# Performance work log

Hardware: AMD Instinct MI355X
Metric: run time of the kernel (lower is better)

## Reference

```python
import jax, jax.numpy as jnp
import numpy as np

N = 1024
BATCH = 256


def setup_inputs() -> dict:
    key = jax.random.key(0)
    k1, k2 = jax.random.split(key)
    log_alpha = jax.random.normal(k1, (BATCH, N), dtype=jnp.float32)
    W = jax.random.normal(k2, (N, N), dtype=jnp.float32)  # unnormalized transition matrix
    return {"log_alpha": log_alpha, "W": W}


def reference(log_alpha, W):
    # log_softmax over dim=0 (columns are distributions over next state)
    log_T = jax.nn.log_softmax(W, axis=0)  # [N, N]
    # log_domain_matmul: out[i, m] = logsumexp_j( log_T[i, j] + log_alpha[m, j] )
    # then transpose back -> out[m, i]
    # broadcast-add cube [BATCH, N, N] then logsumexp over j (tropical-semiring matmul)
    out = jax.scipy.special.logsumexp(
        log_T[None, :, :] + log_alpha[:, None, :], axis=2
    )  # [BATCH, N]
    return out
```

## Files before the change

kernel.cpp:

```cpp
#include <hip/hip_runtime.h>
#include <hip/hip_bf16.h>

#define N 1024
#define BATCH 256
#define NSLAB 16

typedef __attribute__((ext_vector_type(8))) short short8;
typedef __attribute__((ext_vector_type(8))) float f32x8;
typedef __attribute__((ext_vector_type(4))) float f32x4;

static __device__ __forceinline__ ushort bfbits(float f) {
    union { __hip_bfloat16 h; ushort u; } cv;
    cv.h = __float2bfloat16(f);
    return cv.u;
}
static __device__ __forceinline__ float bf2f(ushort u) {
    union { ushort u; __hip_bfloat16 h; } cv;
    cv.u = u;
    return __bfloat162float(cv.h);
}

__global__ __launch_bounds__(256) void k1_psplit(const float* __restrict__ W,
                                                 float* __restrict__ psum,
                                                 __hip_bfloat16* __restrict__ Ph,
                                                 __hip_bfloat16* __restrict__ Pl) {
    const int t    = threadIdx.x;
    const int jg   = blockIdx.x & 15;
    const int slab = blockIdx.x >> 4;
    const int j    = jg * 64 + (t & 63);
    const int rb   = slab * 64 + (t >> 6);

    float acc = 0.f;
#pragma unroll 4
    for (int it = 0; it < 16; ++it) {
        const int i   = rb + it * 4;
        const float e = __expf(W[i * N + j]);
        const __hip_bfloat16 h = __float2bfloat16(e);
        Ph[i * N + j] = h;
        Pl[i * N + j] = __float2bfloat16(e - __bfloat162float(h));
        acc += e;
    }
    __shared__ float sm[256];
    sm[t] = acc;
    __syncthreads();
    if (t < 64)
        psum[slab * N + j] = sm[t] + sm[t + 64] + sm[t + 128] + sm[t + 192];
}

__global__ __launch_bounds__(256) void k3_fused(const float* __restrict__ la,
                                                const float* __restrict__ psum,
                                                const ushort* __restrict__ Ph,
                                                const ushort* __restrict__ Pl,
                                                float* __restrict__ out) {
    __shared__ float  lcs[N];
    __shared__ ushort sQh[32 * 72], sQl[32 * 72], sPh[32 * 72], sPl[32 * 72];

    const int t    = threadIdx.x;
    const int m0   = (blockIdx.x >> 5) * 32;
    const int i0   = (blockIdx.x & 31) * 32;
    const int lane = t & 63;
    const int wid  = t >> 6;
    const int wm   = wid >> 1;
    const int wn   = wid & 1;

#pragma unroll
    for (int jj = 0; jj < 4; ++jj) {
        const int j = jj * 256 + t;
        float cs = 0.f;
#pragma unroll
        for (int s = 0; s < NSLAB; ++s) cs += psum[s * N + j];
        lcs[j] = __logf(cs);
    }
    __syncthreads();

    const int srow = t >> 3;
    const int skc  = (t & 7) * 8;
    const float*  gla = la + (m0 + srow) * N + skc;
    const ushort* gPh = Ph + (i0 + srow) * N + skc;
    const ushort* gPl = Pl + (i0 + srow) * N + skc;
    const int sdst = srow * 72 + skc;

    const int frow = lane & 15;
    const int fkb  = (lane >> 4) * 8;
    const int aoff = (wm * 16 + frow) * 72 + fkb;
    const int boff = (wn * 16 + frow) * 72 + fkb;

    f32x4 acc = {0.f, 0.f, 0.f, 0.f};

    f32x8 vla = *(const f32x8*)(gla);
    short8 vph = *(const short8*)(gPh);
    short8 vpl = *(const short8*)(gPl);

    for (int k0 = 0; k0 < N; k0 += 64) {
        short8 qh, ql;
#pragma unroll
        for (int x = 0; x < 8; ++x) {
            const float q  = __expf(vla[x] - lcs[k0 + skc + x]);
            const ushort h = bfbits(q);
            qh[x] = (short)h;
            ql[x] = (short)bfbits(q - bf2f(h));
        }
        __syncthreads();
        *(short8*)&sQh[sdst] = qh;
        *(short8*)&sQl[sdst] = ql;
        *(short8*)&sPh[sdst] = vph;
        *(short8*)&sPl[sdst] = vpl;
        if (k0 + 64 < N) {
            vla = *(const f32x8*)(gla + k0 + 64);
            vph = *(const short8*)(gPh + k0 + 64);
            vpl = *(const short8*)(gPl + k0 + 64);
        }
        __syncthreads();
#pragma unroll
        for (int ks = 0; ks < 2; ++ks) {
            const short8 aQh = *(const short8*)&sQh[aoff + ks * 32];
            const short8 aQl = *(const short8*)&sQl[aoff + ks * 32];
            const short8 bPh = *(const short8*)&sPh[boff + ks * 32];
            const short8 bPl = *(const short8*)&sPl[boff + ks * 32];
            acc = __builtin_amdgcn_mfma_f32_16x16x32_bf16(aQh, bPh, acc, 0, 0, 0);
            acc = __builtin_amdgcn_mfma_f32_16x16x32_bf16(aQh, bPl, acc, 0, 0, 0);
            acc = __builtin_amdgcn_mfma_f32_16x16x32_bf16(aQl, bPh, acc, 0, 0, 0);
        }
    }

    const int om = m0 + wm * 16 + (lane >> 4) * 4;
    const int oi = i0 + wn * 16 + (lane & 15);
#pragma unroll
    for (int r = 0; r < 4; ++r)
        out[(om + r) * N + oi] = __logf(acc[r]);
}

extern "C" void kernel_launch(void* const* d_in, const int* in_sizes, int n_in,
                              void* d_out, int out_size, void* d_ws, size_t ws_size,
                              hipStream_t stream) {
    const float* la = (const float*)d_in[0];
    const float* W  = (const float*)d_in[1];
    float* out = (float*)d_out;

    char* ws = (char*)d_ws;
    float* psum        = (float*)ws;
    __hip_bfloat16* Ph = (__hip_bfloat16*)(ws + (64 << 10));
    __hip_bfloat16* Pl = Ph + (size_t)N * N;

    k1_psplit<<<256, 256, 0, stream>>>(W, psum, Ph, Pl);
    k3_fused<<<256, 256, 0, stream>>>(la, psum,
                                      (const ushort*)Ph, (const ushort*)Pl, out);
}
```

Before: 72.76 us.

## Split Q precompute into separate kernel and use split-K matmul with 512 threads

Moves the column-sum log and exp/bf16 hi-lo split of log_alpha out of the matmul kernel into a new k2_qsplit kernel, so each Q element is computed once instead of being recomputed by every i-block. The matmul kernel now loads precomputed bf16 Q tiles, uses 128-wide K tiles with 8 waves split across two K halves, and reduces the partial sums through shared memory. k1 is vectorized to 4-wide loads and stores with 16-row slabs. The cost is an extra kernel launch, an extra global round trip for Qh/Ql, and a 64-way psum reduction in k2.

```diff
diff --git a/kernel.cpp b/kernel.cpp
--- a/kernel.cpp
+++ b/kernel.cpp
@@ -3,112 +3,142 @@
 
 #define N 1024
 #define BATCH 256
-#define NSLAB 16
+#define LPAD 136
 
+typedef __attribute__((ext_vector_type(4))) short short4v;
 typedef __attribute__((ext_vector_type(8))) short short8;
-typedef __attribute__((ext_vector_type(8))) float f32x8;
 typedef __attribute__((ext_vector_type(4))) float f32x4;
 
 static __device__ __forceinline__ ushort bfbits(float f) {
-    union { __hip_bfloat16 h; ushort u; } cv;
-    cv.h = __float2bfloat16(f);
-    return cv.u;
+    union { __hip_bfloat16 h; ushort u; } cv; cv.h = __float2bfloat16(f); return cv.u;
 }
 static __device__ __forceinline__ float bf2f(ushort u) {
-    union { ushort u; __hip_bfloat16 h; } cv;
-    cv.u = u;
-    return __bfloat162float(cv.h);
+    union { ushort u; __hip_bfloat16 h; } cv; cv.u = u; return __bfloat162float(cv.h);
 }
 
 __global__ __launch_bounds__(256) void k1_psplit(const float* __restrict__ W,
                                                  float* __restrict__ psum,
-                                                 __hip_bfloat16* __restrict__ Ph,
-                                                 __hip_bfloat16* __restrict__ Pl) {
-    const int t    = threadIdx.x;
-    const int jg   = blockIdx.x & 15;
-    const int slab = blockIdx.x >> 4;
-    const int j    = jg * 64 + (t & 63);
-    const int rb   = slab * 64 + (t >> 6);
-
-    float acc = 0.f;
-#pragma unroll 4
-    for (int it = 0; it < 16; ++it) {
-        const int i   = rb + it * 4;
-        const float e = __expf(W[i * N + j]);
-        const __hip_bfloat16 h = __float2bfloat16(e);
-        Ph[i * N + j] = h;
-        Pl[i * N + j] = __float2bfloat16(e - __bfloat162float(h));
+                                                 ushort* __restrict__ Ph,
+                                                 ushort* __restrict__ Pl) {
+    const int t = threadIdx.x, lane = t & 63, w = t >> 6;
+    const int cg = blockIdx.x & 3, slab = blockIdx.x >> 2;
+    const int c = cg * 256 + lane * 4;
+    __shared__ f32x4 sm[4][64];
+    f32x4 acc = {0.f, 0.f, 0.f, 0.f};
+#pragma unroll
+    for (int it = 0; it < 4; ++it) {
+        const int row = slab * 16 + w * 4 + it;
+        const f32x4 v = *(const f32x4*)(W + row * N + c);
+        short4v ph, pl;
+        f32x4 e;
+#pragma unroll
+        for (int x = 0; x < 4; ++x) {
+            e[x] = __expf(v[x]);
+            const ushort h = bfbits(e[x]);
+            ph[x] = (short)h;
+            pl[x] = (short)bfbits(e[x] - bf2f(h));
+        }
+        *(short4v*)(Ph + row * N + c) = ph;
+        *(short4v*)(Pl + row * N + c) = pl;
         acc += e;
     }
-    __shared__ float sm[256];
-    sm[t] = acc;
+    sm[w][lane] = acc;
     __syncthreads();
     if (t < 64)
-        psum[slab * N + j] = sm[t] + sm[t + 64] + sm[t + 128] + sm[t + 192];
+        *(f32x4*)(psum + slab * N + c) =
+            sm[0][lane] + sm[1][lane] + sm[2][lane] + sm[3][lane];
 }
 
-__global__ __launch_bounds__(256) void k3_fused(const float* __restrict__ la,
-                                                const float* __restrict__ psum,
-                                                const ushort* __restrict__ Ph,
-                                                const ushort* __restrict__ Pl,
-                                                float* __restrict__ out) {
-    __shared__ float  lcs[N];
-    __shared__ ushort sQh[32 * 72], sQl[32 * 72], sPh[32 * 72], sPl[32 * 72];
+__global__ __launch_bounds__(256) void k2_qsplit(const float* __restrict__ la,
+                                                 const float* __restrict__ psum,
+                                                 ushort* __restrict__ Qh,
+                                                 ushort* __restrict__ Ql) {
+    const int t = threadIdx.x;
+    const int cg = blockIdx.x & 7, mg = blockIdx.x >> 3;
+    const int c0 = cg * 128;
+    __shared__ f32x4 smred[8][32];
+    __shared__ float lcs[128];
 
-    const int t    = threadIdx.x;
-    const int m0   = (blockIdx.x >> 5) * 32;
-    const int i0   = (blockIdx.x & 31) * 32;
-    const int lane = t & 63;
-    const int wid  = t >> 6;
-    const int wm   = wid >> 1;
-    const int wn   = wid & 1;
-
+    const int q = t & 31, sg = t >> 5;
+    f32x4 a = {0.f, 0.f, 0.f, 0.f};
 #pragma unroll
-    for (int jj = 0; jj < 4; ++jj) {
-        const int j = jj * 256 + t;
-        float cs = 0.f;
+    for (int i = 0; i < 8; ++i)
+        a += *(const f32x4*)(psum + (sg * 8 + i) * N + c0 + q * 4);
+    smred[sg][q] = a;
+    __syncthreads();
+    if (t < 32) {
+        f32x4 s = {0.f, 0.f, 0.f, 0.f};
 #pragma unroll
-        for (int s = 0; s < NSLAB; ++s) cs += psum[s * N + j];
-        lcs[j] = __logf(cs);
+        for (int g = 0; g < 8; ++g) s += smred[g][t];
+#pragma unroll
+        for (int x = 0; x < 4; ++x) lcs[t * 4 + x] = __logf(s[x]);
     }
     __syncthreads();
 
-    const int srow = t >> 3;
-    const int skc  = (t & 7) * 8;
-    const float*  gla = la + (m0 + srow) * N + skc;
+    const int row = mg * 16 + (t >> 4);
+    const int cc  = (t & 15) * 8;
+    const float* pla = la + row * N + c0 + cc;
+    const f32x4 v0 = *(const f32x4*)(pla);
+    const f32x4 v1 = *(const f32x4*)(pla + 4);
+    short8 qh, ql;
+#pragma unroll
+    for (int x = 0; x < 8; ++x) {
+        const float lv = (x < 4) ? v0[x] : v1[x - 4];
+        const float qv = __expf(lv - lcs[cc + x]);
+        const ushort h = bfbits(qv);
+        qh[x] = (short)h;
+        ql[x] = (short)bfbits(qv - bf2f(h));
+    }
+    *(short8*)(Qh + row * N + c0 + cc) = qh;
+    *(short8*)(Ql + row * N + c0 + cc) = ql;
+}
+
+__global__ __launch_bounds__(512) void k3_mm(const ushort* __restrict__ Qh,
+                                             const ushort* __restrict__ Ql,
+                                             const ushort* __restrict__ Ph,
+                                             const ushort* __restrict__ Pl,
+                                             float* __restrict__ out) {
+    __shared__ ushort sQh[32 * LPAD], sQl[32 * LPAD];
+    __shared__ ushort sPh[32 * LPAD], sPl[32 * LPAD];
+
+    const int t    = threadIdx.x;
+    const int lane = t & 63;
+    const int wid  = t >> 6;
+    const int wm   = (wid >> 1) & 1;
+    const int wn   = wid & 1;
+    const int g    = wid >> 2;
+    const int m0   = (blockIdx.x >> 5) * 32;
+    const int i0   = (blockIdx.x & 31) * 32;
+
+    const int srow = t >> 4;
+    const int skc  = (t & 15) * 8;
+    const ushort* gQh = Qh + (m0 + srow) * N + skc;
+    const ushort* gQl = Ql + (m0 + srow) * N + skc;
     const ushort* gPh = Ph + (i0 + srow) * N + skc;
     const ushort* gPl = Pl + (i0 + srow) * N + skc;
-    const int sdst = srow * 72 + skc;
+    const int sdst = srow * LPAD + skc;
 
-    const int frow = lane & 15;
-    const int fkb  = (lane >> 4) * 8;
-    const int aoff = (wm * 16 + frow) * 72 + fkb;
-    const int boff = (wn * 16 + frow) * 72 + fkb;
+    const int aoff = (wm * 16 + (lane & 15)) * LPAD + g * 64 + (lane >> 4) * 8;
+    const int boff = (wn * 16 + (lane & 15)) * LPAD + g * 64 + (lane >> 4) * 8;
 
     f32x4 acc = {0.f, 0.f, 0.f, 0.f};
 
-    f32x8 vla = *(const f32x8*)(gla);
+    short8 vqh = *(const short8*)(gQh);
+    short8 vql = *(const short8*)(gQl);
     short8 vph = *(const short8*)(gPh);
     short8 vpl = *(const short8*)(gPl);
 
-    for (int k0 = 0; k0 < N; k0 += 64) {
-        short8 qh, ql;
-#pragma unroll
-        for (int x = 0; x < 8; ++x) {
-            const float q  = __expf(vla[x] - lcs[k0 + skc + x]);
-            const ushort h = bfbits(q);
-            qh[x] = (short)h;
-            ql[x] = (short)bfbits(q - bf2f(h));
-        }
+    for (int k0 = 0; k0 < N; k0 += 128) {
         __syncthreads();
-        *(short8*)&sQh[sdst] = qh;
-        *(short8*)&sQl[sdst] = ql;
+        *(short8*)&sQh[sdst] = vqh;
+        *(short8*)&sQl[sdst] = vql;
         *(short8*)&sPh[sdst] = vph;
         *(short8*)&sPl[sdst] = vpl;
-        if (k0 + 64 < N) {
-            vla = *(const f32x8*)(gla + k0 + 64);
-            vph = *(const short8*)(gPh + k0 + 64);
-            vpl = *(const short8*)(gPl + k0 + 64);
+        if (k0 + 128 < N) {
+            vqh = *(const short8*)(gQh + k0 + 128);
+            vql = *(const short8*)(gQl + k0 + 128);
+            vph = *(const short8*)(gPh + k0 + 128);
+            vpl = *(const short8*)(gPl + k0 + 128);
         }
         __syncthreads();
 #pragma unroll
@@ -123,11 +153,18 @@
         }
     }
 
-    const int om = m0 + wm * 16 + (lane >> 4) * 4;
-    const int oi = i0 + wn * 16 + (lane & 15);
+    __syncthreads();
+    f32x4* red = (f32x4*)sQh;
+    red[wid * 64 + lane] = acc;
+    __syncthreads();
+    if (wid < 4) {
+        const f32x4 s = red[wid * 64 + lane] + red[(wid + 4) * 64 + lane];
+        const int om = m0 + wm * 16 + (lane >> 4) * 4;
+        const int oi = i0 + wn * 16 + (lane & 15);
 #pragma unroll
-    for (int r = 0; r < 4; ++r)
-        out[(om + r) * N + oi] = __logf(acc[r]);
+        for (int r = 0; r < 4; ++r)
+            out[(om + r) * N + oi] = __logf(s[r]);
+    }
 }
 
 extern "C" void kernel_launch(void* const* d_in, const int* in_sizes, int n_in,
@@ -138,11 +175,13 @@
     float* out = (float*)d_out;
 
     char* ws = (char*)d_ws;
-    float* psum        = (float*)ws;
-    __hip_bfloat16* Ph = (__hip_bfloat16*)(ws + (64 << 10));
-    __hip_bfloat16* Pl = Ph + (size_t)N * N;
+    float*  psum = (float*)ws;
+    ushort* Ph   = (ushort*)(ws + (256 << 10));
+    ushort* Pl   = Ph + (size_t)N * N;
+    ushort* Qh   = Pl + (size_t)N * N;
+    ushort* Ql   = Qh + (size_t)BATCH * N;
 
     k1_psplit<<<256, 256, 0, stream>>>(W, psum, Ph, Pl);
-    k3_fused<<<256, 256, 0, stream>>>(la, psum,
-                                      (const ushort*)Ph, (const ushort*)Pl, out);
+    k2_qsplit<<<128, 256, 0, stream>>>(la, psum, Qh, Ql);
+    k3_mm<<<256, 512, 0, stream>>>(Qh, Ql, Ph, Pl, out);
 }
```

New measurement: 68.65 us. 5.6% less time.
